# Kernel optimization log

Hardware: AMD Instinct MI355X
Metric: run time of the kernel (lower is better)

Reference implementation:

```python
import jax, jax.numpy as jnp
import numpy as np

N_EMBD = 500
BLOCK_SIZE = 256


def _rope(q, k, theta=0.0001):
    # Faithful to the torch code: freq exponent uses the FULL dim C, and the
    # tensor is split into contiguous halves (not interleaved pairs).
    B, T, C = q.shape
    half = C // 2
    i = jnp.arange(half)
    freqs = theta ** (2.0 * (i // 2).astype(q.dtype) / C)  # [half]
    ang = jnp.arange(T, dtype=q.dtype)[:, None] * freqs[None, :]  # [T, half]
    cos_p, sin_p = jnp.cos(ang), jnp.sin(ang)
    q1, q2 = q[..., :half], q[..., half:]
    k1, k2 = k[..., :half], k[..., half:]
    q_rot = jnp.concatenate([q1 * cos_p - q2 * sin_p, q1 * sin_p + q2 * cos_p], axis=-1)
    k_rot = jnp.concatenate([k1 * cos_p - k2 * sin_p, k1 * sin_p + k2 * cos_p], axis=-1)
    return q_rot, k_rot


def setup_inputs() -> dict:
    key = jax.random.key(0)
    k1, k2, k3, k4 = jax.random.split(key, 4)
    B, T = 256, 256
    scale = 1.0 / np.sqrt(N_EMBD)
    x = jax.random.normal(k1, (B, T, N_EMBD), dtype=jnp.float32)
    Wq = jax.random.normal(k2, (N_EMBD, 500), dtype=jnp.float32) * scale
    Wk = jax.random.normal(k3, (N_EMBD, 500), dtype=jnp.float32) * scale
    Wv = jax.random.normal(k4, (N_EMBD, 500), dtype=jnp.float32) * scale
    return {"x": x, "Wq": Wq, "Wk": Wk, "Wv": Wv}


def reference(x, Wq, Wk, Wv):
    B, T, C = x.shape  # C == n_embd == 500
    q = jnp.einsum("btc,ch->bth", x, Wq)
    k = jnp.einsum("btc,ch->bth", x, Wk)
    q, k = _rope(q, k)
    # NOTE: original scales by input-dim C**-0.5 (500), not head_size**-0.5.
    wei = jnp.einsum("bth,bsh->bts", q, k) * (C ** -0.5)
    causal = jnp.tril(jnp.ones((T, T), dtype=bool))
    wei = jnp.where(causal, wei, -jnp.inf)
    wei = jax.nn.softmax(wei, axis=-1)
    # dropout: eval mode (identity) for deterministic reference
    v = jnp.einsum("btc,ch->bth", x, Wv)
    return jnp.einsum("bts,bsh->bth", wei, v)
```

## Files before the change

kernel.cpp:

```cpp
#include <hip/hip_runtime.h>

typedef unsigned short u16;
typedef __attribute__((ext_vector_type(8))) __bf16 bf16x8;
typedef __attribute__((ext_vector_type(4))) float f32x4;

__device__ __forceinline__ float bf2f(u16 u) {
  union { unsigned int i; float f; } v; v.i = ((unsigned int)u) << 16; return v.f;
}
__device__ __forceinline__ u16 f2bf(float f) {
  union { float f; unsigned int i; } v; v.f = f;
  unsigned int u = v.i;
  return (u16)((u + 0x7fffu + ((u >> 16) & 1u)) >> 16);
}
__device__ __forceinline__ void async16(void* lds, const void* g) {
  __builtin_amdgcn_global_load_lds(
      (const __attribute__((address_space(1))) unsigned int*)g,
      (__attribute__((address_space(3))) unsigned int*)lds, 16, 0, 0);
}

__global__ void k_convert_x(const float* __restrict__ x, u16* __restrict__ xb) {
  int idx = blockIdx.x * 256 + threadIdx.x;
  int m = idx >> 9, c = idx & 511;
  float v = (c < 500) ? x[(size_t)m * 500 + c] : 0.f;
  xb[idx] = f2bf(v);
}

__global__ void k_convert_w(const float* __restrict__ Wq, const float* __restrict__ Wk,
                            const float* __restrict__ Wv, u16* __restrict__ Wt) {
  int idx = blockIdx.x * 256 + threadIdx.x;
  int g = idx >> 18;
  int r = idx & 262143;
  int n = r >> 9, k = r & 511;
  const float* W = (g == 0) ? Wq : (g == 1) ? Wk : Wv;
  int orig = (g == 2) ? n : ((n & 1) ? (n >> 1) + 250 : (n >> 1));
  float v = (n < 500 && k < 500) ? W[(size_t)k * 500 + orig] : 0.f;
  Wt[idx] = f2bf(v);
}

__global__ void k_tables(float* __restrict__ cospair, float* __restrict__ sinpair) {
  int t = blockIdx.x, p = threadIdx.x;
  float c = 0.f, s = 0.f;
  if (p < 250) {
    float ex = (float)(2 * (p >> 1)) / 500.0f;
    float fr = powf(1e-4f, ex);
    float ang = (float)t * fr;
    c = cosf(ang); s = sinf(ang);
  }
  cospair[t * 256 + p] = c;
  sinpair[t * 256 + p] = s;
}

__global__ __launch_bounds__(256, 2) void k_gemm_qkv(
    const u16* __restrict__ xb, const u16* __restrict__ Wt,
    const float* __restrict__ cospair, const float* __restrict__ sinpair,
    u16* __restrict__ qb, u16* __restrict__ kb, u16* __restrict__ vT) {
  __shared__ u16 As[4][128][64];
  const int tid = threadIdx.x;
  const int lane = tid & 63;
  const int w = tid >> 6;
  const int wm = w >> 1, wn = w & 1;
  const int lrow = lane & 15, lhi = lane >> 4;
  const int sx = lrow & 7;

  int bid = blockIdx.x;
  int wk = (bid & 7) * 384 + (bid >> 3);
  int mg = wk / 24;
  int j24 = wk - mg * 24;
  int g = j24 >> 3, bni = j24 & 7;
  const int bn = bni << 6;
  const int m0 = mg << 9;

  const u16* Ab = xb + (size_t)m0 * 512;

  bf16x8 breg[8][2][2];
  {
    const u16* Bl = Wt + ((size_t)(g * 512 + bn + wn * 32) + lrow) * 512 + lhi * 8;
#pragma unroll
    for (int t = 0; t < 8; ++t)
#pragma unroll
      for (int ni = 0; ni < 2; ++ni)
#pragma unroll
        for (int kk2 = 0; kk2 < 2; ++kk2)
          breg[t][ni][kk2] =
              *(const bf16x8*)(Bl + (size_t)ni * 16 * 512 + t * 64 + kk2 * 32);
  }

#define STAGE(S) { int mt_ = (S) >> 3, t_ = (S) & 7, buf_ = (S) & 3;          \
    _Pragma("unroll")                                                         \
    for (int ld = 0; ld < 4; ++ld) {                                          \
      int gi = ld * 256 + tid;                                                \
      int r_ = gi >> 3, c_ = gi & 7;                                          \
      async16((char*)As + buf_ * 16384 + (size_t)gi * 16,                     \
              Ab + ((size_t)(mt_ * 128 + r_)) * 512 + t_ * 64 +               \
                  ((c_ ^ (r_ & 7)) * 8));                                     \
    } }

#define AFRAGS(T)                                                             \
    const u16* Asl = (const u16*)As + ((T) & 3) * 8192;                       \
    bf16x8 a[4][2];                                                           \
    _Pragma("unroll")                                                         \
    for (int mi = 0; mi < 4; ++mi)                                            \
      _Pragma("unroll")                                                       \
      for (int kk2 = 0; kk2 < 2; ++kk2)                                       \
        a[mi][kk2] = *(const bf16x8*)(Asl + (wm * 64 + mi * 16 + lrow) * 64 + \
                                      (((kk2 * 4 + lhi) ^ sx) * 8));

#define EPILOGUE(MT) {                                                        \
    int mb = m0 + (MT) * 128;                                                 \
    if (g < 2) {                                                              \
      u16* dst = (g == 0) ? qb : kb;                                          \
      _Pragma("unroll")                                                       \
      for (int mi = 0; mi < 4; ++mi)                                          \
        _Pragma("unroll")                                                     \
        for (int ni = 0; ni < 2; ++ni) {                                      \
          int n = bn + wn * 32 + ni * 16 + lrow;                              \
          int p = n >> 1;                                                     \
          _Pragma("unroll")                                                   \
          for (int jj = 0; jj < 4; ++jj) {                                    \
            int m = mb + wm * 64 + mi * 16 + lhi * 4 + jj;                    \
            float v = acc[mi][ni][jj];                                        \
            float o = __shfl_xor(v, 1, 64);                                   \
            int ti = (m & 255) * 256 + p;                                     \
            float c = cospair[ti], s = sinpair[ti];                           \
            float r = (n & 1) ? (o * s + v * c) : (v * c - o * s);            \
            dst[(size_t)m * 512 + n] = f2bf(r);                               \
          }                                                                   \
        }                                                                     \
    } else {                                                                  \
      _Pragma("unroll")                                                       \
      for (int mi = 0; mi < 4; ++mi)                                          \
        _Pragma("unroll")                                                     \
        for (int ni = 0; ni < 2; ++ni) {                                      \
          int n = bn + wn * 32 + ni * 16 + lrow;                              \
          _Pragma("unroll")                                                   \
          for (int jj = 0; jj < 4; ++jj) {                                    \
            int m = mb + wm * 64 + mi * 16 + lhi * 4 + jj;                    \
            vT[(size_t)(m >> 8) * 131072 + (size_t)n * 256 + (m & 255)] =     \
                f2bf(acc[mi][ni][jj]);                                        \
          }                                                                   \
        }                                                                     \
    } }

  STAGE(0); STAGE(1); STAGE(2);
  asm volatile("s_waitcnt vmcnt(8)" ::: "memory");
  __builtin_amdgcn_s_barrier();
  asm volatile("" ::: "memory");

  for (int mt = 0; mt < 3; ++mt) {
    f32x4 acc[4][2] = {};
#pragma unroll
    for (int t = 0; t < 8; ++t) {
      STAGE(mt * 8 + t + 3);
      AFRAGS(t);
      __builtin_amdgcn_s_setprio(1);
#pragma unroll
      for (int kk2 = 0; kk2 < 2; ++kk2)
#pragma unroll
        for (int mi = 0; mi < 4; ++mi)
#pragma unroll
          for (int ni = 0; ni < 2; ++ni)
            acc[mi][ni] = __builtin_amdgcn_mfma_f32_16x16x32_bf16(
                a[mi][kk2], breg[t][ni][kk2], acc[mi][ni], 0, 0, 0);
      __builtin_amdgcn_s_setprio(0);
      asm volatile("s_waitcnt vmcnt(8)" ::: "memory");
      __builtin_amdgcn_s_barrier();
      asm volatile("" ::: "memory");
    }
    EPILOGUE(mt);
  }
  {
    f32x4 acc[4][2] = {};
#pragma unroll
    for (int t = 0; t < 8; ++t) {
      if (t < 5) STAGE(27 + t);
      AFRAGS(t);
      __builtin_amdgcn_s_setprio(1);
#pragma unroll
      for (int kk2 = 0; kk2 < 2; ++kk2)
#pragma unroll
        for (int mi = 0; mi < 4; ++mi)
#pragma unroll
          for (int ni = 0; ni < 2; ++ni)
            acc[mi][ni] = __builtin_amdgcn_mfma_f32_16x16x32_bf16(
                a[mi][kk2], breg[t][ni][kk2], acc[mi][ni], 0, 0, 0);
      __builtin_amdgcn_s_setprio(0);
      if (t < 5)      asm volatile("s_waitcnt vmcnt(8)" ::: "memory");
      else if (t == 5) asm volatile("s_waitcnt vmcnt(4)" ::: "memory");
      else if (t == 6) asm volatile("s_waitcnt vmcnt(0)" ::: "memory");
      if (t < 7) {
        __builtin_amdgcn_s_barrier();
        asm volatile("" ::: "memory");
      }
    }
    EPILOGUE(3);
  }
#undef STAGE
#undef AFRAGS
#undef EPILOGUE
}

__global__ __launch_bounds__(256) void k_attn(
    const u16* __restrict__ qb, const u16* __restrict__ kb,
    const u16* __restrict__ vT, float* __restrict__ out) {
  __shared__ u16 smem[32768];
  u16* Ks = smem;
  u16* Ps = smem + 16384;
  u16* Vs = smem;

  const int tid = threadIdx.x;
  const int lane = tid & 63;
  const int w = tid >> 6;
  int bid = blockIdx.x;
  int wk = (bid & 7) * 128 + (bid >> 3);
  const int b = wk >> 2;
  const int t0 = (wk & 3) * 64;
  const int smax = t0 + 63;
  const int lrow = lane & 15, lhi = lane >> 4;
  const int sx = lrow & 7;
  const int vxor = (lrow >> 1) & 3;

  const u16* qrow = qb + ((size_t)(b * 256 + t0 + w * 16 + lrow)) * 512;
  bf16x8 qf[16];
#pragma unroll
  for (int kk = 0; kk < 16; ++kk)
    qf[kk] = *(const bf16x8*)(qrow + kk * 32 + lhi * 8);

  f32x4 sa[16] = {};
#pragma unroll
  for (int st = 0; st < 8; ++st) {
    const int s0 = st * 32;
    if (s0 <= smax) {
      __syncthreads();
#pragma unroll
      for (int it = 0; it < 8; ++it) {
        int gi = it * 256 + tid;
        int r = gi >> 6;
        int sl = (gi & 63) ^ (r & 7);
        async16(Ks + (size_t)gi * 8, kb + ((size_t)(b * 256 + s0 + r)) * 512 + sl * 8);
      }
      __syncthreads();
      __builtin_amdgcn_s_setprio(1);
#pragma unroll
      for (int ni = 0; ni < 2; ++ni)
#pragma unroll
        for (int kk = 0; kk < 16; ++kk) {
          bf16x8 bf = *(const bf16x8*)&Ks[(ni * 16 + lrow) * 512 + ((kk * 4 + lhi) ^ sx) * 8];
          sa[st * 2 + ni] =
              __builtin_amdgcn_mfma_f32_16x16x32_bf16(qf[kk], bf, sa[st * 2 + ni], 0, 0, 0);
        }
      __builtin_amdgcn_s_setprio(0);
    }
  }

  const float scale = 0.04472135954999579f;
  float rmax[4] = {-1e30f, -1e30f, -1e30f, -1e30f};
#pragma unroll
  for (int n = 0; n < 16; ++n) {
    int s = n * 16 + lrow;
#pragma unroll
    for (int j = 0; j < 4; ++j) {
      int t = t0 + w * 16 + lhi * 4 + j;
      float v = sa[n][j] * scale;
      if (s > t) v = -1e30f;
      sa[n][j] = v;
      rmax[j] = fmaxf(rmax[j], v);
    }
  }
#pragma unroll
  for (int j = 0; j < 4; ++j)
#pragma unroll
    for (int msk = 1; msk < 16; msk <<= 1)
      rmax[j] = fmaxf(rmax[j], __shfl_xor(rmax[j], msk, 64));
  float rsum[4] = {0.f, 0.f, 0.f, 0.f};
#pragma unroll
  for (int n = 0; n < 16; ++n)
#pragma unroll
    for (int j = 0; j < 4; ++j) {
      float p = __expf(sa[n][j] - rmax[j]);
      sa[n][j] = p;
      rsum[j] += p;
    }
#pragma unroll
  for (int j = 0; j < 4; ++j)
#pragma unroll
    for (int msk = 1; msk < 16; msk <<= 1)
      rsum[j] += __shfl_xor(rsum[j], msk, 64);
  float rinv[4];
#pragma unroll
  for (int j = 0; j < 4; ++j) rinv[j] = 1.0f / rsum[j];

#pragma unroll
  for (int n = 0; n < 16; ++n)
#pragma unroll
    for (int j = 0; j < 4; ++j) {
      int s = n * 16 + lrow;
      int trow = w * 16 + lhi * 4 + j;
      int slot = (s >> 3) ^ (trow & 7);
      Ps[trow * 256 + slot * 8 + (s & 7)] = f2bf(sa[n][j] * rinv[j]);
    }

  f32x4 o[32] = {};
#pragma unroll
  for (int st = 0; st < 8; ++st) {
    const int s0 = st * 32;
    if (s0 <= smax) {
      __syncthreads();
#pragma unroll
      for (int it = 0; it < 8; ++it) {
        int gi = it * 256 + tid;
        int r = gi >> 2;
        int sl = (gi & 3) ^ ((r >> 1) & 3);
        async16(Vs + (size_t)gi * 8, vT + (size_t)b * 131072 + (size_t)r * 256 + s0 + sl * 8);
      }
      __syncthreads();
      bf16x8 pf = *(const bf16x8*)&Ps[(w * 16 + lrow) * 256 + (((st * 4) + lhi) ^ sx) * 8];
      __builtin_amdgcn_s_setprio(1);
#pragma unroll
      for (int ni = 0; ni < 32; ++ni) {
        bf16x8 vf = *(const bf16x8*)&Vs[(ni * 16 + lrow) * 32 + ((lhi ^ vxor) * 8)];
        o[ni] = __builtin_amdgcn_mfma_f32_16x16x32_bf16(pf, vf, o[ni], 0, 0, 0);
      }
      __builtin_amdgcn_s_setprio(0);
    }
  }

  const int tb = t0 + w * 16;
#pragma unroll
  for (int ni = 0; ni < 32; ++ni) {
    int h = ni * 16 + lrow;
    if (h < 500) {
#pragma unroll
      for (int j = 0; j < 4; ++j) {
        int t = tb + lhi * 4 + j;
        out[((size_t)(b * 256 + t)) * 500 + h] = o[ni][j];
      }
    }
  }
}

extern "C" void kernel_launch(void* const* d_in, const int* in_sizes, int n_in,
                              void* d_out, int out_size, void* d_ws, size_t ws_size,
                              hipStream_t stream) {
  const float* x  = (const float*)d_in[0];
  const float* Wq = (const float*)d_in[1];
  const float* Wk = (const float*)d_in[2];
  const float* Wv = (const float*)d_in[3];
  float* out = (float*)d_out;

  u16* xb = (u16*)d_ws;
  u16* qb = xb + 33554432;
  u16* kb = qb + 33554432;
  u16* vT = kb + 33554432;
  u16* Wt = vT + 33554432;
  float* cospair = (float*)(Wt + 786432);
  float* sinpair = cospair + 65536;

  k_convert_x<<<131072, 256, 0, stream>>>(x, xb);
  k_convert_w<<<3072, 256, 0, stream>>>(Wq, Wk, Wv, Wt);
  k_tables<<<256, 256, 0, stream>>>(cospair, sinpair);
  k_gemm_qkv<<<3072, 256, 0, stream>>>(xb, Wt, cospair, sinpair, qb, kb, vT);
  k_attn<<<1024, 256, 0, stream>>>(qb, kb, vT, out);
}
```

Measured before the change: 374.2 us.

## Pipeline attention K/V loads through a triple-buffered LDS ring; vectorize x conversion

The attention kernel now streams K tiles of 16 rows and V half-tiles through a three-slot LDS ring with async loads issued two stages ahead. It synchronises with explicit vmcnt waits and barriers in place of a pair of __syncthreads per stage, so global loads overlap MFMA work. The x-to-bf16 conversion is also changed to write 8 elements per thread with a single 16-byte store, launching an eighth as many blocks. The larger LDS footprint (80KB) may reduce occupancy, and the hand-counted waits must exactly match the issued loads.

```diff
diff --git a/kernel.cpp b/kernel.cpp
--- a/kernel.cpp
+++ b/kernel.cpp
@@ -20,9 +20,14 @@
 
 __global__ void k_convert_x(const float* __restrict__ x, u16* __restrict__ xb) {
   int idx = blockIdx.x * 256 + threadIdx.x;
-  int m = idx >> 9, c = idx & 511;
-  float v = (c < 500) ? x[(size_t)m * 500 + c] : 0.f;
-  xb[idx] = f2bf(v);
+  int m = idx >> 6, c0 = (idx & 63) * 8;
+  u16 o[8];
+#pragma unroll
+  for (int j = 0; j < 8; ++j) {
+    int c = c0 + j;
+    o[j] = f2bf((c < 500) ? x[(size_t)m * 500 + c] : 0.f);
+  }
+  *(uint4*)(xb + (size_t)m * 512 + c0) = *(const uint4*)o;
 }
 
 __global__ void k_convert_w(const float* __restrict__ Wq, const float* __restrict__ Wk,
@@ -95,8 +100,8 @@
                   ((c_ ^ (r_ & 7)) * 8));                                     \
     } }
 
-#define AFRAGS(T)                                                             \
-    const u16* Asl = (const u16*)As + ((T) & 3) * 8192;                       \
+#define AFRAGS(S)                                                             \
+    const u16* Asl = (const u16*)As + ((S) & 3) * 8192;                       \
     bf16x8 a[4][2];                                                           \
     _Pragma("unroll")                                                         \
     for (int mi = 0; mi < 4; ++mi)                                            \
@@ -202,22 +207,24 @@
 __global__ __launch_bounds__(256) void k_attn(
     const u16* __restrict__ qb, const u16* __restrict__ kb,
     const u16* __restrict__ vT, float* __restrict__ out) {
-  __shared__ u16 smem[32768];
-  u16* Ks = smem;
-  u16* Ps = smem + 16384;
-  u16* Vs = smem;
+  __shared__ u16 smem[40960];
+  u16* Ring = smem;
+  u16* Ps = smem + 24576;
 
   const int tid = threadIdx.x;
   const int lane = tid & 63;
   const int w = tid >> 6;
   int bid = blockIdx.x;
-  int wk = (bid & 7) * 128 + (bid >> 3);
-  const int b = wk >> 2;
-  const int t0 = (wk & 3) * 64;
-  const int smax = t0 + 63;
+  int wkk = (bid & 7) * 128 + (bid >> 3);
+  const int b = wkk >> 2;
+  const int qt = wkk & 3;
+  const int t0 = qt * 64;
   const int lrow = lane & 15, lhi = lane >> 4;
   const int sx = lrow & 7;
   const int vxor = (lrow >> 1) & 3;
+  const int NT = 4 * (qt + 1);
+  const int NTB = 2 * (qt + 1);
+  const int NV = 2 * NTB;
 
   const u16* qrow = qb + ((size_t)(b * 256 + t0 + w * 16 + lrow)) * 512;
   bf16x8 qf[16];
@@ -225,30 +232,49 @@
   for (int kk = 0; kk < 16; ++kk)
     qf[kk] = *(const bf16x8*)(qrow + kk * 32 + lhi * 8);
 
+#define STAGE_K(ST) {                                                         \
+    _Pragma("unroll")                                                         \
+    for (int ld = 0; ld < 4; ++ld) {                                          \
+      int gi = ld * 256 + tid;                                                \
+      int r_ = gi >> 6, c_ = gi & 63;                                         \
+      async16((char*)Ring + ((ST) % 3) * 16384 + (size_t)gi * 16,             \
+              kb + ((size_t)(b * 256 + (ST) * 16 + r_)) * 512 +               \
+                  ((c_ ^ (r_ & 7)) * 8));                                     \
+    } }
+
+#define STAGE_V(ST, HH) {                                                     \
+    _Pragma("unroll")                                                         \
+    for (int ld = 0; ld < 4; ++ld) {                                          \
+      int gi = ld * 256 + tid;                                                \
+      int r_ = gi >> 2, c_ = gi & 3;                                          \
+      async16((char*)Ring + (((ST) * 2 + (HH)) % 3) * 16384 + (size_t)gi * 16,\
+              vT + (size_t)b * 131072 + ((size_t)((HH) * 256 + r_)) * 256 +   \
+                  (ST) * 32 + ((c_ ^ ((r_ >> 1) & 3)) * 8));                  \
+    } }
+
   f32x4 sa[16] = {};
-#pragma unroll
-  for (int st = 0; st < 8; ++st) {
-    const int s0 = st * 32;
-    if (s0 <= smax) {
-      __syncthreads();
-#pragma unroll
-      for (int it = 0; it < 8; ++it) {
-        int gi = it * 256 + tid;
-        int r = gi >> 6;
-        int sl = (gi & 63) ^ (r & 7);
-        async16(Ks + (size_t)gi * 8, kb + ((size_t)(b * 256 + s0 + r)) * 512 + sl * 8);
+  STAGE_K(0); STAGE_K(1);
+  asm volatile("s_waitcnt vmcnt(4)" ::: "memory");
+  __builtin_amdgcn_s_barrier();
+  asm volatile("" ::: "memory");
+#pragma unroll
+  for (int st = 0; st < 16; ++st) {
+    if (st < NT) {
+      if (st + 2 < NT) STAGE_K(st + 2);
+      const u16* Ksl = Ring + (st % 3) * 8192 + lrow * 512;
+      __builtin_amdgcn_s_setprio(1);
+#pragma unroll
+      for (int kk = 0; kk < 16; ++kk) {
+        bf16x8 bf = *(const bf16x8*)(Ksl + ((kk * 4 + lhi) ^ sx) * 8);
+        sa[st] = __builtin_amdgcn_mfma_f32_16x16x32_bf16(qf[kk], bf, sa[st], 0, 0, 0);
       }
-      __syncthreads();
-      __builtin_amdgcn_s_setprio(1);
-#pragma unroll
-      for (int ni = 0; ni < 2; ++ni)
-#pragma unroll
-        for (int kk = 0; kk < 16; ++kk) {
-          bf16x8 bf = *(const bf16x8*)&Ks[(ni * 16 + lrow) * 512 + ((kk * 4 + lhi) ^ sx) * 8];
-          sa[st * 2 + ni] =
-              __builtin_amdgcn_mfma_f32_16x16x32_bf16(qf[kk], bf, sa[st * 2 + ni], 0, 0, 0);
-        }
       __builtin_amdgcn_s_setprio(0);
+      if (st + 2 < NT)      asm volatile("s_waitcnt vmcnt(4)" ::: "memory");
+      else if (st + 1 < NT) asm volatile("s_waitcnt vmcnt(0)" ::: "memory");
+      if (st + 1 < NT) {
+        __builtin_amdgcn_s_barrier();
+        asm volatile("" ::: "memory");
+      }
     }
   }
 
@@ -299,43 +325,57 @@
       Ps[trow * 256 + slot * 8 + (s & 7)] = f2bf(sa[n][j] * rinv[j]);
     }
 
-  f32x4 o[32] = {};
+  __syncthreads();
+
+  f32x4 o[2][16] = {};
+  STAGE_V(0, 0); STAGE_V(0, 1);
+  asm volatile("s_waitcnt vmcnt(4)" ::: "memory");
+  __builtin_amdgcn_s_barrier();
+  asm volatile("" ::: "memory");
 #pragma unroll
   for (int st = 0; st < 8; ++st) {
-    const int s0 = st * 32;
-    if (s0 <= smax) {
-      __syncthreads();
-#pragma unroll
-      for (int it = 0; it < 8; ++it) {
-        int gi = it * 256 + tid;
-        int r = gi >> 2;
-        int sl = (gi & 3) ^ ((r >> 1) & 3);
-        async16(Vs + (size_t)gi * 8, vT + (size_t)b * 131072 + (size_t)r * 256 + s0 + sl * 8);
+    if (st < NTB) {
+#pragma unroll
+      for (int hh = 0; hh < 2; ++hh) {
+        const int f = st * 2 + hh;
+        if (f + 2 < NV) {
+          if (hh == 0) STAGE_V(st + 1, 0) else STAGE_V(st + 1, 1);
+        }
+        bf16x8 pf = *(const bf16x8*)&Ps[(w * 16 + lrow) * 256 + ((st * 4 + lhi) ^ sx) * 8];
+        const u16* Vsl = Ring + (f % 3) * 8192;
+        __builtin_amdgcn_s_setprio(1);
+#pragma unroll
+        for (int ni = 0; ni < 16; ++ni) {
+          bf16x8 vf = *(const bf16x8*)(Vsl + (ni * 16 + lrow) * 32 + (lhi ^ vxor) * 8);
+          o[hh][ni] = __builtin_amdgcn_mfma_f32_16x16x32_bf16(pf, vf, o[hh][ni], 0, 0, 0);
+        }
+        __builtin_amdgcn_s_setprio(0);
+        if (f + 2 < NV)      asm volatile("s_waitcnt vmcnt(4)" ::: "memory");
+        else if (f + 1 < NV) asm volatile("s_waitcnt vmcnt(0)" ::: "memory");
+        if (f + 1 < NV) {
+          __builtin_amdgcn_s_barrier();
+          asm volatile("" ::: "memory");
+        }
       }
-      __syncthreads();
-      bf16x8 pf = *(const bf16x8*)&Ps[(w * 16 + lrow) * 256 + (((st * 4) + lhi) ^ sx) * 8];
-      __builtin_amdgcn_s_setprio(1);
-#pragma unroll
-      for (int ni = 0; ni < 32; ++ni) {
-        bf16x8 vf = *(const bf16x8*)&Vs[(ni * 16 + lrow) * 32 + ((lhi ^ vxor) * 8)];
-        o[ni] = __builtin_amdgcn_mfma_f32_16x16x32_bf16(pf, vf, o[ni], 0, 0, 0);
+    }
+  }
+#undef STAGE_K
+#undef STAGE_V
+
+  const int tb = t0 + w * 16;
+#pragma unroll
+  for (int hh = 0; hh < 2; ++hh)
+#pragma unroll
+    for (int ni = 0; ni < 16; ++ni) {
+      int h = hh * 256 + ni * 16 + lrow;
+      if (h < 500) {
+#pragma unroll
+        for (int j = 0; j < 4; ++j) {
+          int t = tb + lhi * 4 + j;
+          out[((size_t)(b * 256 + t)) * 500 + h] = o[hh][ni][j];
+        }
       }
-      __builtin_amdgcn_s_setprio(0);
-    }
-  }
-
-  const int tb = t0 + w * 16;
-#pragma unroll
-  for (int ni = 0; ni < 32; ++ni) {
-    int h = ni * 16 + lrow;
-    if (h < 500) {
-#pragma unroll
-      for (int j = 0; j < 4; ++j) {
-        int t = tb + lhi * 4 + j;
-        out[((size_t)(b * 256 + t)) * 500 + h] = o[ni][j];
-      }
-    }
-  }
+    }
 }
 
 extern "C" void kernel_launch(void* const* d_in, const int* in_sizes, int n_in,
@@ -355,7 +395,7 @@
   float* cospair = (float*)(Wt + 786432);
   float* sinpair = cospair + 65536;
 
-  k_convert_x<<<131072, 256, 0, stream>>>(x, xb);
+  k_convert_x<<<16384, 256, 0, stream>>>(x, xb);
   k_convert_w<<<3072, 256, 0, stream>>>(Wq, Wk, Wv, Wt);
   k_tables<<<256, 256, 0, stream>>>(cospair, sinpair);
   k_gemm_qkv<<<3072, 256, 0, stream>>>(xb, Wt, cospair, sinpair, qb, kb, vT);
```

Measured after the change: 349.5 us, median of 2. 1.07x faster.
